# Performance work log

Hardware: AMD Instinct MI355X
Metric: run time of the kernel (lower is better)

The kernel has to match this reference:

```python
import jax, jax.numpy as jnp
import numpy as np

# Static problem dims (all graphs equal-sized so adaptive pool = uniform bins)
B = 64          # graphs
N = 2048        # nodes per graph
E = 16          # node_emb_dim
H_OUT, W_OUT = 32, 4   # AdaptiveAvgPool2d output -> pooled_dim = 128
COND = 64       # cond_emb_dim
HID = 512       # mlp_h_dim
BN_EPS = 1e-5


def _lin_init(key, out_d, in_d):
    kw, kb = jax.random.split(key)
    lim = 1.0 / np.sqrt(in_d)
    W = jax.random.uniform(kw, (out_d, in_d), jnp.float32, -lim, lim)
    b = jax.random.uniform(kb, (out_d,), jnp.float32, -lim, lim)
    return W, b


def setup_inputs() -> dict:
    key = jax.random.key(0)
    ks = jax.random.split(key, 6)
    Ntot = B * N
    x = jax.random.normal(ks[0], (Ntot, E), jnp.float32)
    batch = jnp.repeat(jnp.arange(B, dtype=jnp.int32), N)  # sorted segment ids
    cond = jax.random.normal(ks[1], (Ntot, COND), jnp.float32)
    mlp_in = COND + H_OUT * W_OUT  # 192
    W1, b1 = _lin_init(ks[2], HID, mlp_in)
    W2, b2 = _lin_init(ks[3], HID, HID)
    W3, b3 = _lin_init(ks[4], 3, HID)
    g1 = jnp.ones((HID,), jnp.float32); be1 = jnp.zeros((HID,), jnp.float32)
    g2 = jnp.ones((HID,), jnp.float32); be2 = jnp.zeros((HID,), jnp.float32)
    return {"x": x, "batch": batch, "conditioner_z_ref": cond,
            "W1": W1, "b1": b1, "g1": g1, "be1": be1,
            "W2": W2, "b2": b2, "g2": g2, "be2": be2,
            "W3": W3, "b3": b3}


def _bn_gelu(h, g, be):
    # BatchNorm1d in training mode: biased batch stats over the node axis
    m = h.mean(axis=0)
    v = h.var(axis=0)
    h = g * (h - m) * jax.lax.rsqrt(v + BN_EPS) + be
    return jax.nn.gelu(h, approximate=False)


def reference(x, batch, conditioner_z_ref, W1, b1, g1, be1, W2, b2, g2, be2, W3, b3):
    # Per-graph adaptive avg pool: since N % H_OUT == 0 and E % W_OUT == 0,
    # AdaptiveAvgPool2d is exactly mean over uniform (N/H_OUT, E/W_OUT) bins.
    xb = x.reshape(B, H_OUT, N // H_OUT, W_OUT, E // W_OUT)
    batch_pooled = xb.mean(axis=(2, 4)).reshape(B, H_OUT * W_OUT)  # [B, 128]
    pooled_per_node = batch_pooled[batch]                           # gather to [Ntot, 128]
    h = jnp.concatenate([conditioner_z_ref, pooled_per_node], axis=1)  # [Ntot, 192]
    h = _bn_gelu(h @ W1.T + b1, g1, be1)
    h = _bn_gelu(h @ W2.T + b2, g2, be2)
    return h @ W3.T + b3  # [Ntot, 3] predicted coords
```

## Files before the change

kernel.cpp:

```cpp
#include <hip/hip_runtime.h>
#include <hip/hip_bf16.h>
#include <math.h>
#include <stdint.h>

#define B_GRAPHS 64
#define N_NODES  2048
#define E_DIM    16
#define M_TOT    (B_GRAPHS * N_NODES)
#define K_COND   64
#define MLP_IN   192
#define HID      512
#define POOLD    128
#define BN_EPS   1e-5f

typedef __attribute__((ext_vector_type(8))) short bfrag8;
typedef __attribute__((ext_vector_type(4))) float facc4;

__device__ __forceinline__ unsigned short f2b(float f) {
    unsigned int x = __builtin_bit_cast(unsigned int, f);
    unsigned int r = x + 0x7fffu + ((x >> 16) & 1u);
    return (unsigned short)(r >> 16);
}
__device__ __forceinline__ float b2f(unsigned short u) {
    unsigned int x = ((unsigned int)u) << 16;
    return __builtin_bit_cast(float, x);
}

__device__ __forceinline__ float gelu_fast(float y) {
    float x  = y * 0.70710678118654752440f;
    float ax = fabsf(x);
    float t  = __builtin_amdgcn_rcpf(fmaf(0.3275911f, ax, 1.0f));
    float p  = fmaf(1.061405429f, t, -1.453152027f);
    p = fmaf(p, t, 1.421413741f);
    p = fmaf(p, t, -0.284496736f);
    p = fmaf(p, t, 0.254829592f);
    p = p * t;
    float e = __expf(-x * x);
    float erfax = fmaf(-p, e, 1.0f);
    float erfx  = copysignf(erfax, x);
    return 0.5f * y * (1.0f + erfx);
}

#define GLOAD_LDS16(g, l)                                                        \
    __builtin_amdgcn_global_load_lds(                                            \
        (const __attribute__((address_space(1))) unsigned int*)(const void*)(g), \
        (__attribute__((address_space(3))) unsigned int*)(void*)(l), 16, 0, 0)

__global__ __launch_bounds__(512) void prep_kernel(const float* __restrict__ x,
                                                   const float* __restrict__ W1,
                                                   const float* __restrict__ b1,
                                                   float* __restrict__ gbias) {
    __shared__ float pl[POOLD];
    int g = blockIdx.x, t = threadIdx.x;
    if (t < 128) {
        int h = t >> 2, w = t & 3;
        const float* base = x + (size_t)g * N_NODES * E_DIM + (size_t)h * 64 * E_DIM + w * 4;
        float s = 0.f;
        #pragma unroll 4
        for (int r = 0; r < 64; ++r) {
            float4 v = *reinterpret_cast<const float4*>(base + (size_t)r * E_DIM);
            s += v.x + v.y + v.z + v.w;
        }
        pl[h * 4 + w] = s * (1.0f / 256.0f);
    }
    __syncthreads();
    const float* wr_ = W1 + (size_t)t * MLP_IN + K_COND;
    float s = b1[t];
    #pragma unroll 4
    for (int k = 0; k < POOLD; ++k) s = fmaf(pl[k], wr_[k], s);
    gbias[g * HID + t] = s;
}

__global__ __launch_bounds__(256) void cvt_kernel(const float* __restrict__ s,
                                                  unsigned short* __restrict__ d) {
    size_t i = ((size_t)blockIdx.x * 256 + threadIdx.x) * 8;
    float4 v0 = *reinterpret_cast<const float4*>(s + i);
    float4 v1 = *reinterpret_cast<const float4*>(s + i + 4);
    unsigned short t[8] = {f2b(v0.x), f2b(v0.y), f2b(v0.z), f2b(v0.w),
                           f2b(v1.x), f2b(v1.y), f2b(v1.z), f2b(v1.w)};
    *reinterpret_cast<bfrag8*>(d + i) = *reinterpret_cast<bfrag8*>(t);
}

__device__ __forceinline__ bfrag8 load_f32x8_as_bf16(const float* p) {
    float4 v0 = *reinterpret_cast<const float4*>(p);
    float4 v1 = *reinterpret_cast<const float4*>(p + 4);
    unsigned short t[8] = {f2b(v0.x), f2b(v0.y), f2b(v0.z), f2b(v0.w),
                           f2b(v1.x), f2b(v1.y), f2b(v1.z), f2b(v1.w)};
    return *reinterpret_cast<bfrag8*>(t);
}

__global__ __launch_bounds__(512, 1) void gemm1_kernel(const float* __restrict__ A,
                                                       const float* __restrict__ W,
                                                       const float* __restrict__ gbias,
                                                       float* __restrict__ sums,
                                                       unsigned short* __restrict__ C) {
    __shared__ unsigned short As[128 * 64];
    __shared__ float sArr[HID], qArr[HID];
    const int t = threadIdx.x;
    const int r0 = blockIdx.x * 128;
    const int g = r0 >> 11;
    const int l = t & 63, w = t >> 6;
    const int wr = w >> 2, wc = w & 3;
    const int ln = l & 15, kg = l >> 4;
    sArr[t] = 0.f; qArr[t] = 0.f;

    {
        const int cg = t & 7, rb = t >> 3;
        #pragma unroll
        for (int i = 0; i < 2; ++i) {
            int row = rb + i * 64;
            bfrag8 vv = load_f32x8_as_bf16(A + (size_t)(r0 + row) * K_COND + cg * 8);
            int dg = row * 8 + (cg ^ (row & 7));
            *reinterpret_cast<bfrag8*>(&As[dg * 8]) = vv;
        }
    }
    bfrag8 bf0[8], bf1[8];
    #pragma unroll
    for (int b = 0; b < 8; ++b) {
        int RB = wc * 128 + b * 16 + ln;
        bf0[b] = load_f32x8_as_bf16(W + (size_t)RB * MLP_IN + kg * 8);
        bf1[b] = load_f32x8_as_bf16(W + (size_t)RB * MLP_IN + 32 + kg * 8);
    }
    __syncthreads();

    facc4 acc[4][8];
    const facc4 z = {0.f, 0.f, 0.f, 0.f};
    #pragma unroll
    for (int a = 0; a < 4; ++a)
        #pragma unroll
        for (int b = 0; b < 8; ++b) acc[a][b] = z;

    #pragma unroll
    for (int s = 0; s < 2; ++s) {
        bfrag8 af[4];
        #pragma unroll
        for (int a = 0; a < 4; ++a) {
            int RA = wr * 64 + a * 16 + ln;
            af[a] = *reinterpret_cast<const bfrag8*>(&As[(RA * 8 + ((s * 4 + kg) ^ (RA & 7))) * 8]);
        }
        #pragma unroll
        for (int a = 0; a < 4; ++a)
            #pragma unroll
            for (int b = 0; b < 8; ++b)
                acc[a][b] = __builtin_amdgcn_mfma_f32_16x16x32_bf16(
                    af[a], s == 0 ? bf0[b] : bf1[b], acc[a][b], 0, 0, 0);
    }

    const float* gb = gbias + (size_t)g * HID;
    float gbv[8];
    #pragma unroll
    for (int b = 0; b < 8; ++b) gbv[b] = gb[wc * 128 + b * 16 + ln];
    float cs[8], cq[8];
    #pragma unroll
    for (int b = 0; b < 8; ++b) { cs[b] = 0.f; cq[b] = 0.f; }
    #pragma unroll
    for (int a = 0; a < 4; ++a) {
        #pragma unroll
        for (int i = 0; i < 4; ++i) {
            size_t rbase = (size_t)(r0 + wr * 64 + a * 16 + kg * 4 + i) * HID + wc * 128 + ln;
            #pragma unroll
            for (int b = 0; b < 8; ++b) {
                float v = acc[a][b][i] + gbv[b];
                C[rbase + b * 16] = f2b(v);
                cs[b] += v; cq[b] = fmaf(v, v, cq[b]);
            }
        }
    }
    #pragma unroll
    for (int b = 0; b < 8; ++b) {
        cs[b] += __shfl_xor(cs[b], 16, 64); cq[b] += __shfl_xor(cq[b], 16, 64);
        cs[b] += __shfl_xor(cs[b], 32, 64); cq[b] += __shfl_xor(cq[b], 32, 64);
    }
    if (kg == 0) {
        #pragma unroll
        for (int b = 0; b < 8; ++b) {
            int cl = wc * 128 + b * 16 + ln;
            atomicAdd(&sArr[cl], cs[b]); atomicAdd(&qArr[cl], cq[b]);
        }
    }
    __syncthreads();
    atomicAdd(&sums[t], sArr[t]);
    atomicAdd(&sums[HID + t], qArr[t]);
}

__global__ void finalize_kernel(const float* __restrict__ sums, const float* __restrict__ g,
                                const float* __restrict__ be, float* __restrict__ ss) {
    int n = threadIdx.x;
    float mean = sums[n] * (1.0f / M_TOT);
    float var = sums[HID + n] * (1.0f / M_TOT) - mean * mean;
    float sc = g[n] * rsqrtf(var + BN_EPS);
    ss[n] = sc;
    ss[HID + n] = be[n] - mean * sc;
}

__global__ __launch_bounds__(256) void act_kernel(unsigned short* __restrict__ H,
                                                  const float* __restrict__ ss) {
    size_t idx = ((size_t)blockIdx.x * 256 + threadIdx.x) * 8;
    int col = (int)(idx & (HID - 1));
    bfrag8 v = *reinterpret_cast<bfrag8*>(&H[idx]);
    #pragma unroll
    for (int j = 0; j < 8; ++j) {
        float x = b2f((unsigned short)v[j]);
        float y = fmaf(x, ss[col + j], ss[HID + col + j]);
        y = gelu_fast(y);
        v[j] = (short)f2b(y);
    }
    *reinterpret_cast<bfrag8*>(&H[idx]) = v;
}

__global__ __launch_bounds__(256) void gemm2_kernel(const unsigned short* __restrict__ A,
                                                    const unsigned short* __restrict__ Bm,
                                                    const float* __restrict__ bias,
                                                    float* __restrict__ sums,
                                                    unsigned short* __restrict__ C) {
    __shared__ unsigned short As[128 * 32];
    __shared__ unsigned short Bs[128 * 32];
    __shared__ float sArr[128], qArr[128];
    const int d = blockIdx.x;
    const int xcd = d & 7, slot = d >> 3;
    const int cb = slot & 3, rhi = slot >> 2;
    const int rb = (rhi << 3) | xcd;
    const int r0 = rb * 128, c0 = cb * 128;
    const int t = threadIdx.x;
    const int l = t & 63, w = t >> 6;
    const int wr = w >> 1, wc = w & 1;
    const int ln = l & 15, kg = l >> 4;
    const int rr = l >> 2, sp = l & 3;
    const int bss = sp ^ ((rr >> 1) & 3);
    if (t < 128) { sArr[t] = 0.f; qArr[t] = 0.f; }

    facc4 acc[4][4];
    const facc4 z = {0.f, 0.f, 0.f, 0.f};
    #pragma unroll
    for (int a = 0; a < 4; ++a)
        #pragma unroll
        for (int b = 0; b < 4; ++b) acc[a][b] = z;

    for (int kk = 0; kk < HID; kk += 32) {
        #pragma unroll
        for (int c = 0; c < 2; ++c) {
            const int chunk = w * 2 + c;
            const unsigned short* ga = A + (size_t)(r0 + chunk * 16 + rr) * HID + kk + bss * 8;
            GLOAD_LDS16(ga, &As[chunk * 512]);
            const unsigned short* gb = Bm + (size_t)(c0 + chunk * 16 + rr) * HID + kk + bss * 8;
            GLOAD_LDS16(gb, &Bs[chunk * 512]);
        }
        __syncthreads();
        bfrag8 af[4], bf[4];
        #pragma unroll
        for (int a = 0; a < 4; ++a) {
            int RA = wr * 64 + a * 16 + ln;
            af[a] = *reinterpret_cast<const bfrag8*>(&As[RA * 32 + (kg ^ ((RA >> 1) & 3)) * 8]);
        }
        #pragma unroll
        for (int b = 0; b < 4; ++b) {
            int RB = wc * 64 + b * 16 + ln;
            bf[b] = *reinterpret_cast<const bfrag8*>(&Bs[RB * 32 + (kg ^ ((RB >> 1) & 3)) * 8]);
        }
        #pragma unroll
        for (int a = 0; a < 4; ++a)
            #pragma unroll
            for (int b = 0; b < 4; ++b)
                acc[a][b] = __builtin_amdgcn_mfma_f32_16x16x32_bf16(af[a], bf[b], acc[a][b], 0, 0, 0);
        __syncthreads();
    }

    float bb[4];
    #pragma unroll
    for (int b = 0; b < 4; ++b) bb[b] = bias[c0 + wc * 64 + b * 16 + ln];
    float cs[4] = {0.f, 0.f, 0.f, 0.f}, cq[4] = {0.f, 0.f, 0.f, 0.f};
    #pragma unroll
    for (int a = 0; a < 4; ++a) {
        #pragma unroll
        for (int i = 0; i < 4; ++i) {
            size_t rbase = (size_t)(r0 + wr * 64 + a * 16 + kg * 4 + i) * HID + c0 + wc * 64 + ln;
            #pragma unroll
            for (int b = 0; b < 4; ++b) {
                float v = acc[a][b][i] + bb[b];
                C[rbase + b * 16] = f2b(v);
                cs[b] += v; cq[b] = fmaf(v, v, cq[b]);
            }
        }
    }
    #pragma unroll
    for (int b = 0; b < 4; ++b) {
        cs[b] += __shfl_xor(cs[b], 16, 64); cq[b] += __shfl_xor(cq[b], 16, 64);
        cs[b] += __shfl_xor(cs[b], 32, 64); cq[b] += __shfl_xor(cq[b], 32, 64);
    }
    if (kg == 0) {
        #pragma unroll
        for (int b = 0; b < 4; ++b) {
            int cl = wc * 64 + b * 16 + ln;
            atomicAdd(&sArr[cl], cs[b]); atomicAdd(&qArr[cl], cq[b]);
        }
    }
    __syncthreads();
    if (t < 128) {
        atomicAdd(&sums[c0 + t], sArr[t]);
        atomicAdd(&sums[HID + c0 + t], qArr[t]);
    }
}

__global__ __launch_bounds__(256) void g3_kernel(const unsigned short* __restrict__ H2,
                                                 const float* __restrict__ ss2,
                                                 const float* __restrict__ W3,
                                                 const float* __restrict__ b3,
                                                 float* __restrict__ out) {
    __shared__ float lss[2 * HID];
    __shared__ float lw3[3 * HID];
    int t = threadIdx.x;
    for (int i = t; i < 2 * HID; i += 256) lss[i] = ss2[i];
    for (int i = t; i < 3 * HID; i += 256) lw3[i] = W3[i];
    __syncthreads();
    int l = t & 63, w = t >> 6;
    int rsub = l >> 3, lk = l & 7;
    int row = blockIdx.x * 32 + w * 8 + rsub;
    const unsigned short* p = H2 + (size_t)row * HID;
    float o0 = 0.f, o1 = 0.f, o2 = 0.f;
    #pragma unroll
    for (int it = 0; it < 8; ++it) {
        int k = it * 64 + lk * 8;
        bfrag8 v = *reinterpret_cast<const bfrag8*>(p + k);
        #pragma unroll
        for (int j = 0; j < 8; ++j) {
            float x = b2f((unsigned short)v[j]);
            float y = fmaf(x, lss[k + j], lss[HID + k + j]);
            y = gelu_fast(y);
            o0 = fmaf(y, lw3[k + j], o0);
            o1 = fmaf(y, lw3[HID + k + j], o1);
            o2 = fmaf(y, lw3[2 * HID + k + j], o2);
        }
    }
    #pragma unroll
    for (int m = 1; m < 8; m <<= 1) {
        o0 += __shfl_xor(o0, m, 64);
        o1 += __shfl_xor(o1, m, 64);
        o2 += __shfl_xor(o2, m, 64);
    }
    if (lk == 0) {
        out[(size_t)row * 3 + 0] = o0 + b3[0];
        out[(size_t)row * 3 + 1] = o1 + b3[1];
        out[(size_t)row * 3 + 2] = o2 + b3[2];
    }
}

extern "C" void kernel_launch(void* const* d_in, const int* in_sizes, int n_in,
                              void* d_out, int out_size, void* d_ws, size_t ws_size,
                              hipStream_t stream) {
    const float* x     = (const float*)d_in[0];
    const float* cond  = (const float*)d_in[2];
    const float* W1    = (const float*)d_in[3];
    const float* b1    = (const float*)d_in[4];
    const float* g1    = (const float*)d_in[5];
    const float* be1   = (const float*)d_in[6];
    const float* W2    = (const float*)d_in[7];
    const float* b2    = (const float*)d_in[8];
    const float* g2    = (const float*)d_in[9];
    const float* be2   = (const float*)d_in[10];
    const float* W3    = (const float*)d_in[11];
    const float* b3    = (const float*)d_in[12];

    const size_t H_BYTES = (size_t)M_TOT * HID * 2;
    if (ws_size < 2 * H_BYTES) return;
    char* ws = (char*)d_ws;
    unsigned short* H1 = (unsigned short*)ws;
    unsigned short* H2 = (unsigned short*)(ws + H_BYTES);

    float* outf   = (float*)d_out;
    float* gbias  = outf;
    float* sums1  = gbias + B_GRAPHS * HID;
    float* sums2  = sums1 + 2 * HID;
    float* ss1    = sums2 + 2 * HID;
    unsigned short* W2bf = (unsigned short*)(ss1 + 2 * HID);
    float* ss2 = (float*)ws;

    hipMemsetAsync(sums1, 0, 2 * 2 * HID * sizeof(float), stream);

    prep_kernel<<<B_GRAPHS, 512, 0, stream>>>(x, W1, b1, gbias);
    cvt_kernel<<<(HID * HID / 8) / 256, 256, 0, stream>>>(W2, W2bf);

    gemm1_kernel<<<dim3(M_TOT / 128, 1), 512, 0, stream>>>(
        cond, W1, gbias, sums1, H1);
    finalize_kernel<<<1, HID, 0, stream>>>(sums1, g1, be1, ss1);
    act_kernel<<<(M_TOT * HID / 8) / 256, 256, 0, stream>>>(H1, ss1);

    gemm2_kernel<<<(M_TOT / 128) * (HID / 128), 256, 0, stream>>>(
        H1, W2bf, b2, sums2, H2);
    finalize_kernel<<<1, HID, 0, stream>>>(sums2, g2, be2, ss2);

    g3_kernel<<<M_TOT / 32, 256, 0, stream>>>(H2, ss2, W3, b3, outf);
}
```

Measured before the change: 296.7 us.

## Split gemm1 into 128x128 column tiles with XCD-aware mapping; grid-stride act kernel

gemm1 now launches 4096 blocks of 256 threads, each computing a 128x128 output tile, instead of 1024 blocks of 512 threads each covering a full 512-column row slab. Block indices are remapped so that the column tiles of one row block land on the same XCD. This gives more blocks, less register pressure and better occupancy, at the cost of reloading the A tile four times. The activation kernel becomes a grid-stride loop over 2048 blocks that stage the BN scale/shift in shared memory, cutting launch and per-element global lookups of ss.

```diff
diff --git a/kernel.cpp b/kernel.cpp
--- a/kernel.cpp
+++ b/kernel.cpp
@@ -89,46 +89,50 @@
     return *reinterpret_cast<bfrag8*>(t);
 }
 
-__global__ __launch_bounds__(512, 1) void gemm1_kernel(const float* __restrict__ A,
-                                                       const float* __restrict__ W,
-                                                       const float* __restrict__ gbias,
-                                                       float* __restrict__ sums,
-                                                       unsigned short* __restrict__ C) {
+__global__ __launch_bounds__(256) void gemm1_kernel(const float* __restrict__ A,
+                                                    const float* __restrict__ W,
+                                                    const float* __restrict__ gbias,
+                                                    float* __restrict__ sums,
+                                                    unsigned short* __restrict__ C) {
     __shared__ unsigned short As[128 * 64];
-    __shared__ float sArr[HID], qArr[HID];
+    __shared__ float sArr[128], qArr[128];
+    const int d = blockIdx.x;
+    const int xcd = d & 7, slot = d >> 3;
+    const int cb = slot & 3, rhi = slot >> 2;
+    const int rb = (rhi << 3) | xcd;
+    const int r0 = rb * 128, c0 = cb * 128;
+    const int g = r0 >> 11;
     const int t = threadIdx.x;
-    const int r0 = blockIdx.x * 128;
-    const int g = r0 >> 11;
     const int l = t & 63, w = t >> 6;
-    const int wr = w >> 2, wc = w & 3;
+    const int wr = w >> 1, wc = w & 1;
     const int ln = l & 15, kg = l >> 4;
-    sArr[t] = 0.f; qArr[t] = 0.f;
+    if (t < 128) { sArr[t] = 0.f; qArr[t] = 0.f; }
 
     {
-        const int cg = t & 7, rb = t >> 3;
-        #pragma unroll
-        for (int i = 0; i < 2; ++i) {
-            int row = rb + i * 64;
+        const int cg = t & 7, rbase_ = t >> 3;
+        #pragma unroll
+        for (int i = 0; i < 4; ++i) {
+            int row = rbase_ + i * 32;
             bfrag8 vv = load_f32x8_as_bf16(A + (size_t)(r0 + row) * K_COND + cg * 8);
             int dg = row * 8 + (cg ^ (row & 7));
             *reinterpret_cast<bfrag8*>(&As[dg * 8]) = vv;
         }
     }
-    bfrag8 bf0[8], bf1[8];
-    #pragma unroll
-    for (int b = 0; b < 8; ++b) {
-        int RB = wc * 128 + b * 16 + ln;
+    bfrag8 bf0[4], bf1[4];
+    #pragma unroll
+    for (int b = 0; b < 4; ++b) {
+        int RB = c0 + wc * 64 + b * 16 + ln;
         bf0[b] = load_f32x8_as_bf16(W + (size_t)RB * MLP_IN + kg * 8);
         bf1[b] = load_f32x8_as_bf16(W + (size_t)RB * MLP_IN + 32 + kg * 8);
     }
     __syncthreads();
 
-    facc4 acc[4][8];
+    facc4 acc[4][4];
     const facc4 z = {0.f, 0.f, 0.f, 0.f};
     #pragma unroll
     for (int a = 0; a < 4; ++a)
         #pragma unroll
-        for (int b = 0; b < 8; ++b) acc[a][b] = z;
+        for (int b = 0; b < 4; ++b) acc[a][b] = z;
 
     #pragma unroll
     for (int s = 0; s < 2; ++s) {
@@ -141,25 +145,23 @@
         #pragma unroll
         for (int a = 0; a < 4; ++a)
             #pragma unroll
-            for (int b = 0; b < 8; ++b)
+            for (int b = 0; b < 4; ++b)
                 acc[a][b] = __builtin_amdgcn_mfma_f32_16x16x32_bf16(
                     af[a], s == 0 ? bf0[b] : bf1[b], acc[a][b], 0, 0, 0);
     }
 
     const float* gb = gbias + (size_t)g * HID;
-    float gbv[8];
-    #pragma unroll
-    for (int b = 0; b < 8; ++b) gbv[b] = gb[wc * 128 + b * 16 + ln];
-    float cs[8], cq[8];
-    #pragma unroll
-    for (int b = 0; b < 8; ++b) { cs[b] = 0.f; cq[b] = 0.f; }
+    float gbv[4];
+    #pragma unroll
+    for (int b = 0; b < 4; ++b) gbv[b] = gb[c0 + wc * 64 + b * 16 + ln];
+    float cs[4] = {0.f, 0.f, 0.f, 0.f}, cq[4] = {0.f, 0.f, 0.f, 0.f};
     #pragma unroll
     for (int a = 0; a < 4; ++a) {
         #pragma unroll
         for (int i = 0; i < 4; ++i) {
-            size_t rbase = (size_t)(r0 + wr * 64 + a * 16 + kg * 4 + i) * HID + wc * 128 + ln;
+            size_t rbase = (size_t)(r0 + wr * 64 + a * 16 + kg * 4 + i) * HID + c0 + wc * 64 + ln;
             #pragma unroll
-            for (int b = 0; b < 8; ++b) {
+            for (int b = 0; b < 4; ++b) {
                 float v = acc[a][b][i] + gbv[b];
                 C[rbase + b * 16] = f2b(v);
                 cs[b] += v; cq[b] = fmaf(v, v, cq[b]);
@@ -167,20 +169,22 @@
         }
     }
     #pragma unroll
-    for (int b = 0; b < 8; ++b) {
+    for (int b = 0; b < 4; ++b) {
         cs[b] += __shfl_xor(cs[b], 16, 64); cq[b] += __shfl_xor(cq[b], 16, 64);
         cs[b] += __shfl_xor(cs[b], 32, 64); cq[b] += __shfl_xor(cq[b], 32, 64);
     }
     if (kg == 0) {
         #pragma unroll
-        for (int b = 0; b < 8; ++b) {
-            int cl = wc * 128 + b * 16 + ln;
+        for (int b = 0; b < 4; ++b) {
+            int cl = wc * 64 + b * 16 + ln;
             atomicAdd(&sArr[cl], cs[b]); atomicAdd(&qArr[cl], cq[b]);
         }
     }
     __syncthreads();
-    atomicAdd(&sums[t], sArr[t]);
-    atomicAdd(&sums[HID + t], qArr[t]);
+    if (t < 128) {
+        atomicAdd(&sums[c0 + t], sArr[t]);
+        atomicAdd(&sums[HID + c0 + t], qArr[t]);
+    }
 }
 
 __global__ void finalize_kernel(const float* __restrict__ sums, const float* __restrict__ g,
@@ -193,19 +197,30 @@
     ss[HID + n] = be[n] - mean * sc;
 }
 
+#define ACT_BLOCKS 2048
 __global__ __launch_bounds__(256) void act_kernel(unsigned short* __restrict__ H,
                                                   const float* __restrict__ ss) {
-    size_t idx = ((size_t)blockIdx.x * 256 + threadIdx.x) * 8;
-    int col = (int)(idx & (HID - 1));
-    bfrag8 v = *reinterpret_cast<bfrag8*>(&H[idx]);
-    #pragma unroll
-    for (int j = 0; j < 8; ++j) {
-        float x = b2f((unsigned short)v[j]);
-        float y = fmaf(x, ss[col + j], ss[HID + col + j]);
-        y = gelu_fast(y);
-        v[j] = (short)f2b(y);
-    }
-    *reinterpret_cast<bfrag8*>(&H[idx]) = v;
+    __shared__ float lss[2 * HID];
+    int t = threadIdx.x;
+    #pragma unroll
+    for (int i = t; i < 2 * HID; i += 256) lss[i] = ss[i];
+    __syncthreads();
+    size_t gi = (size_t)blockIdx.x * 256 + t;
+    const size_t stride = (size_t)ACT_BLOCKS * 256;
+    #pragma unroll
+    for (int it = 0; it < 16; ++it, gi += stride) {
+        size_t idx = gi * 8;
+        int col = (int)(idx & (HID - 1));
+        bfrag8 v = *reinterpret_cast<bfrag8*>(&H[idx]);
+        #pragma unroll
+        for (int j = 0; j < 8; ++j) {
+            float x = b2f((unsigned short)v[j]);
+            float y = fmaf(x, lss[col + j], lss[HID + col + j]);
+            y = gelu_fast(y);
+            v[j] = (short)f2b(y);
+        }
+        *reinterpret_cast<bfrag8*>(&H[idx]) = v;
+    }
 }
 
 __global__ __launch_bounds__(256) void gemm2_kernel(const unsigned short* __restrict__ A,
@@ -379,10 +394,10 @@
     prep_kernel<<<B_GRAPHS, 512, 0, stream>>>(x, W1, b1, gbias);
     cvt_kernel<<<(HID * HID / 8) / 256, 256, 0, stream>>>(W2, W2bf);
 
-    gemm1_kernel<<<dim3(M_TOT / 128, 1), 512, 0, stream>>>(
+    gemm1_kernel<<<(M_TOT / 128) * (HID / 128), 256, 0, stream>>>(
         cond, W1, gbias, sums1, H1);
     finalize_kernel<<<1, HID, 0, stream>>>(sums1, g1, be1, ss1);
-    act_kernel<<<(M_TOT * HID / 8) / 256, 256, 0, stream>>>(H1, ss1);
+    act_kernel<<<ACT_BLOCKS, 256, 0, stream>>>(H1, ss1);
 
     gemm2_kernel<<<(M_TOT / 128) * (HID / 128), 256, 0, stream>>>(
         H1, W2bf, b2, sums2, H2);
```

After: 296.1 us. About the same (-0.2%).
